# Kernel optimization log

Hardware: AMD Instinct MI355X
Metric: run time of the kernel (lower is better)

The kernel has to match this reference:

```python
import jax, jax.numpy as jnp
import numpy as np

PI = float(np.pi)
C64 = jnp.complex64

# ---- gate matrices (PennyLane conventions) ----

def _rx(t):
    c = jnp.cos(t / 2); s = jnp.sin(t / 2)
    return jnp.array([[c, -1j * s], [-1j * s, c]]).astype(C64)

def _rz(t):
    return jnp.array([[jnp.exp(-0.5j * t), 0.0], [0.0, jnp.exp(0.5j * t)]]).astype(C64)

def _rot(phi, th, om):
    # Rot(phi, theta, omega) = RZ(omega) RY(theta) RZ(phi)
    c = jnp.cos(th / 2); s = jnp.sin(th / 2)
    return jnp.array([
        [jnp.exp(-0.5j * (phi + om)) * c, -jnp.exp(0.5j * (phi - om)) * s],
        [jnp.exp(-0.5j * (phi - om)) * s,  jnp.exp(0.5j * (phi + om)) * c],
    ]).astype(C64)

def _crx(t):
    c = jnp.cos(t / 2); s = jnp.sin(t / 2)
    return jnp.array([
        [1, 0, 0, 0],
        [0, 1, 0, 0],
        [0, 0, c, -1j * s],
        [0, 0, -1j * s, c],
    ]).astype(C64)

CNOT = jnp.array([[1, 0, 0, 0], [0, 1, 0, 0], [0, 0, 0, 1], [0, 0, 1, 0]], dtype=C64)

# ---- state-vector primitives (state shape (2,)*n) ----

def _ap1(psi, U, w):
    return jnp.moveaxis(jnp.tensordot(U, psi, axes=((1,), (w,))), 0, w)

def _ap2(psi, U, a, b):
    U = U.reshape(2, 2, 2, 2)
    return jnp.moveaxis(jnp.tensordot(U, psi, axes=((2, 3), (a, b))), (0, 1), (a, b))

def _expZ(psi, w):
    p = jnp.moveaxis(jnp.abs(psi) ** 2, w, 0)
    return (p[0] - p[1]).sum()

def _expX(psi, w):
    return jnp.real(jnp.sum(jnp.conj(psi) * jnp.flip(psi, axis=w)))

# wire pairs in initQKV_on_wires order
_PAIRS = [(0, 1), (1, 2), (2, 3), (3, 0), (0, 3), (1, 0), (2, 1), (3, 2)]

def _init_qkv(psi, rot_p, crx_p, off):
    for i, (a, b) in enumerate(_PAIRS):
        psi = _ap1(psi, _rot(rot_p[3 * i], rot_p[3 * i + 1], rot_p[3 * i + 2]), off + a)
        psi = _ap2(psi, _crx(crx_p[i]), off + a, off + b)
        psi = _ap2(psi, CNOT, off + a, off + b)
    return psi

def _sample(x, qr, qc, kr, kc, vr, vc):
    # qmha_score: 8-qubit circuit
    psi = jnp.zeros((2,) * 8, C64).at[(0,) * 8].set(1.0)
    for w in range(4):  # AngleEmbedding (RX) of xq
        psi = _ap1(psi, _rx(x[w]), w)
    psi = _init_qkv(psi, qr, qc, 0)
    for w in range(4):  # AngleEmbedding (RX) of xk (same x)
        psi = _ap1(psi, _rx(x[w]), w)
    psi = _init_qkv(psi, kr, kc, 4)
    for w in range(4):
        psi = _ap2(psi, CNOT, w, w + 4)
    z = jnp.stack([_expZ(psi, w) for w in range(4)])
    xm = jnp.stack([_expX(psi, w) for w in range(4)])
    score = jnp.sqrt(z * z + xm * xm)
    # qmha_value: 4-qubit circuit
    phi = jnp.zeros((2,) * 4, C64).at[(0,) * 4].set(1.0)
    for w in range(4):
        phi = _ap1(phi, _rx(x[w]), w)
    phi = _init_qkv(phi, vr, vc, 0)
    for w in range(4):
        phi = _ap1(phi, _rz(jnp.tanh(score[w]) * PI), w)
    for a, b in [(0, 1), (1, 2), (2, 3)]:
        phi = _ap2(phi, CNOT, a, b)
    zv = jnp.stack([_expZ(phi, w) for w in range(4)])
    xv = jnp.stack([_expX(phi, w) for w in range(4)])
    return jnp.concatenate([zv, xv])  # [8]


def setup_inputs() -> dict:
    key = jax.random.key(0)
    ks = jax.random.split(key, 12)
    B = 16384
    u = lambda k, n: jax.random.uniform(k, (n,), jnp.float32, -PI / 2, PI / 2)
    return {
        "x1": jax.random.normal(ks[0], (B, 96), jnp.float32),
        "pre_w": jax.random.normal(ks[1], (4, 96), jnp.float32) / np.sqrt(96.0),
        "pre_b": jnp.zeros((4,), jnp.float32),
        "q_rot": u(ks[2], 24),
        "k_rot": u(ks[3], 24),
        "v_rot": u(ks[4], 24),
        "q_crx": 0.1 * jax.random.normal(ks[5], (8,), jnp.float32),
        "k_crx": 0.1 * jax.random.normal(ks[6], (8,), jnp.float32),
        "v_crx": 0.1 * jax.random.normal(ks[7], (8,), jnp.float32),
        "ln_w": jnp.ones((8,), jnp.float32),
        "ln_b": jnp.zeros((8,), jnp.float32),
        "head_w": jax.random.normal(ks[8], (2, 8), jnp.float32) / np.sqrt(8.0),
        "head_b": jnp.zeros((2,), jnp.float32),
    }


def reference(x1, pre_w, pre_b, q_rot, k_rot, v_rot, q_crx, k_crx, v_crx,
              ln_w, ln_b, head_w, head_b):
    x = x1 @ pre_w.T + pre_b  # [B, 4] angles
    outs = jax.vmap(lambda xi: _sample(xi, q_rot, q_crx, k_rot, k_crx, v_rot, v_crx))(x)  # [B, 8]
    mu = outs.mean(-1, keepdims=True)
    var = outs.var(-1, keepdims=True)
    y = (outs - mu) / jnp.sqrt(var + 1e-5) * ln_w + ln_b  # LayerNorm(8)
    g = jax.nn.gelu(y, approximate=False)  # torch nn.GELU default = exact erf
    return g @ head_w.T + head_b  # [B, 2]
```

## Files before the change

### kernel.cpp

```cpp
#include <hip/hip_runtime.h>
#include <math.h>

#define PI_F 3.14159265358979323846f

struct c32 { float x, y; };


__device__ __forceinline__ void apply_rot_red(c32* s, const int w,
                                              float Ax, float Ay, float Cx, float Cy){
  const int m = 8 >> w;
  #pragma unroll
  for (int i = 0; i < 16; i++){
    if (i & m) continue;
    c32 a = s[i], b = s[i | m];
    s[i].x     = Ax*a.x - Ay*a.y - Cx*b.x - Cy*b.y;
    s[i].y     = Ax*a.y + Ay*a.x - Cx*b.y + Cy*b.x;
    s[i | m].x = Cx*a.x - Cy*a.y + Ax*b.x + Ay*b.y;
    s[i | m].y = Cx*a.y + Cy*a.x + Ax*b.y - Ay*b.x;
  }
}

__device__ __forceinline__ void apply_crxnot(c32* s, const int wa, const int wb,
                                             float c, float sn){
  const int ma = 8 >> wa, mb = 8 >> wb;
  #pragma unroll
  for (int i = 0; i < 16; i++){
    if (!(i & ma) || (i & mb)) continue;
    c32 u = s[i], v = s[i | mb];
    s[i]      = { c*v.x + sn*u.y, c*v.y - sn*u.x };
    s[i | mb] = { c*u.x + sn*v.y, c*u.y - sn*v.x };
  }
}

__device__ __forceinline__ void sim_initqkv(c32* s, const float* gp){
  constexpr int pa[8] = {0,1,2,3,0,1,2,3};
  constexpr int pb[8] = {1,2,3,0,3,0,1,2};
  #pragma unroll
  for (int g = 0; g < 8; g++){
    const float* q = gp + 8*g;
    apply_rot_red(s, pa[g], q[0], q[1], q[2], q[3]);
    apply_crxnot(s, pa[g], pb[g], q[4], q[5]);
  }
}

__device__ __forceinline__ void build_rx(c32* s, const float* cw, const float* sw){
  float m01[4] = { cw[0]*cw[1], cw[0]*sw[1], sw[0]*cw[1], sw[0]*sw[1] };
  float m23[4] = { cw[2]*cw[3], cw[2]*sw[3], sw[2]*cw[3], sw[2]*sw[3] };
  #pragma unroll
  for (int i = 0; i < 16; i++){
    float mag = m01[(i >> 2) & 3] * m23[i & 3];
    const int pc = __popc(i) & 3;
    s[i] = (pc == 0) ? c32{ mag, 0.f } :
           (pc == 1) ? c32{ 0.f, -mag } :
           (pc == 2) ? c32{ -mag, 0.f } : c32{ 0.f, mag };
  }
}

__device__ __forceinline__ float fast_tanh(float x){
  float e = __expf(2.f * x);
  return 1.f - 2.f * __builtin_amdgcn_rcpf(e + 1.f);
}

__global__ __launch_bounds__(64, 1) void qc_setup(
    const float* __restrict__ q_rot, const float* __restrict__ k_rot,
    const float* __restrict__ v_rot,
    const float* __restrict__ q_crx, const float* __restrict__ k_crx,
    const float* __restrict__ v_crx,
    float* __restrict__ ws){

  __shared__ float gates[3 * 64];
  const int t = threadIdx.x;

  if (t < 24){
    const int grp = t >> 3, g = t & 7;
    const float* rotp = grp == 0 ? q_rot : (grp == 1 ? k_rot : v_rot);
    const float* crxp = grp == 0 ? q_crx : (grp == 1 ? k_crx : v_crx);
    float phi = rotp[3*g], th = rotp[3*g+1], om = rotp[3*g+2];
    float c, s, ca, sa, cb, sb;
    __sincosf(0.5f*th,       &s,  &c);
    __sincosf(0.5f*(phi+om), &sa, &ca);
    __sincosf(0.5f*(phi-om), &sb, &cb);
    float cc, cs; __sincosf(0.5f*crxp[g], &cs, &cc);
    float* dst = &gates[64*grp + 8*g];
    dst[0] = c*ca; dst[1] = -c*sa; dst[2] = s*cb; dst[3] = -s*sb;
    dst[4] = cc;   dst[5] = cs;
    dst[6] = 0.f;  dst[7] = 0.f;
  }
  __syncthreads();

  c32 ks[16];
  #pragma unroll
  for (int i = 0; i < 16; i++) ks[i] = { 0.f, 0.f };
  ks[0] = { 1.f, 0.f };
  sim_initqkv(ks, &gates[64]);
  float cxk[4];
  #pragma unroll
  for (int w = 0; w < 4; w++){
    const int m = 8 >> w;
    float r = 0.f;
    #pragma unroll
    for (int i = 0; i < 16; i++){
      if (i & m) continue;
      r += ks[i].x*ks[i|m].x + ks[i].y*ks[i|m].y;
    }
    cxk[w] = 2.f * r;
  }

  ws[t]      = gates[t];
  ws[64 + t] = gates[128 + t];
  if (t < 4) ws[128 + t] = cxk[t];
}

#define LDS_STRIDE 97

__global__ __launch_bounds__(128, 1) void qc_main(
    const float* __restrict__ x1,
    const float* __restrict__ pre_w, const float* __restrict__ pre_b,
    const float* __restrict__ gws,
    const float* __restrict__ ln_w, const float* __restrict__ ln_b,
    const float* __restrict__ head_w, const float* __restrict__ head_b,
    float* __restrict__ out, int B){

  __shared__ float xs[64 * LDS_STRIDE];
  __shared__ float gl[132];
  __shared__ float scr[8][64];

  const int t    = threadIdx.x;
  const int lane = t & 63;
  const int wid  = t >> 6;
  const int base = blockIdx.x * 64;

  if (t < 128) gl[t] = gws[t];
  if (t < 4)   gl[128 + t] = gws[128 + t];

  {
    int rem = B - base; if (rem > 64) rem = 64;
    const int nf4 = rem * 24;
    const float4* src = (const float4*)(x1 + (long)base * 96);
    #pragma unroll
    for (int k = 0; k < 12; k++){
      int g = t + 128*k;
      if (g < nf4){
        float4 v = src[g];
        int f = 4*g;
        int r = f / 96, cidx = f - 96*r;
        float* d = &xs[r*LDS_STRIDE + cidx];
        d[0]=v.x; d[1]=v.y; d[2]=v.z; d[3]=v.w;
      }
    }
  }
  __syncthreads();

  float xw[4];
  {
    float a0 = pre_b[0], a1 = pre_b[1], a2 = pre_b[2], a3 = pre_b[3];
    const float* row = &xs[lane * LDS_STRIDE];
    #pragma unroll
    for (int j = 0; j < 96; j++){
      float v = row[j];
      a0 += v * pre_w[j];
      a1 += v * pre_w[96  + j];
      a2 += v * pre_w[192 + j];
      a3 += v * pre_w[288 + j];
    }
    xw[0]=a0; xw[1]=a1; xw[2]=a2; xw[3]=a3;
  }

  float cw[4], sw[4];
  #pragma unroll
  for (int w = 0; w < 4; w++) __sincosf(0.5f*xw[w], &sw[w], &cw[w]);

  c32 st[16];
  build_rx(st, cw, sw);

  float o[8];

  if (wid == 0){
    sim_initqkv(st, &gl[0]);
    float p[16];
    #pragma unroll
    for (int i = 0; i < 16; i++) p[i] = st[i].x*st[i].x + st[i].y*st[i].y;
    #pragma unroll
    for (int w = 0; w < 4; w++){
      const int m = 8 >> w;
      float sz = 0.f, sx = 0.f, sy = 0.f;
      #pragma unroll
      for (int i = 0; i < 16; i++) sz += (i & m) ? -p[i] : p[i];
      #pragma unroll
      for (int i = 0; i < 16; i++){
        if (i & m) continue;
        c32 a = st[i], b = st[i|m];
        sx += a.x*b.x + a.y*b.y;
        sy += a.x*b.y - a.y*b.x;
      }
      float cth = 1.f - 2.f*sw[w]*sw[w];
      float sth = 2.f*sw[w]*cw[w];
      float z   = cth*sz + sth*(2.f*sy);
      float xm  = (2.f*sx) * gl[128 + w];
      float score = sqrtf(z*z + xm*xm);
      float th = fast_tanh(score) * PI_F;
      float srv, crv; __sincosf(0.5f*th, &srv, &crv);
      scr[2*w][lane]     = crv;
      scr[2*w + 1][lane] = srv;
    }
  } else {
    sim_initqkv(st, &gl[64]);
    float p[16];
    #pragma unroll
    for (int i = 0; i < 16; i++) p[i] = st[i].x*st[i].x + st[i].y*st[i].y;
    constexpr int zm[4] = {8, 12, 14, 15};
    #pragma unroll
    for (int w = 0; w < 4; w++){
      float r = 0.f;
      #pragma unroll
      for (int i = 0; i < 16; i++)
        r += (__popc(i & zm[w]) & 1) ? -p[i] : p[i];
      o[w] = r;
    }
  }

  __syncthreads();

  if (wid == 1){
    float cr[4], sr[4];
    #pragma unroll
    for (int w = 0; w < 4; w++){
      cr[w] = scr[2*w][lane];
      sr[w] = scr[2*w + 1][lane];
    }
    c32 ph01[4], ph23[4];
    ph01[0] = { cr[0]*cr[1] - sr[0]*sr[1], -(cr[0]*sr[1] + sr[0]*cr[1]) };
    ph01[1] = { cr[0]*cr[1] + sr[0]*sr[1],   cr[0]*sr[1] - sr[0]*cr[1] };
    ph01[2] = { ph01[1].x, -ph01[1].y };
    ph01[3] = { ph01[0].x, -ph01[0].y };
    ph23[0] = { cr[2]*cr[3] - sr[2]*sr[3], -(cr[2]*sr[3] + sr[2]*cr[3]) };
    ph23[1] = { cr[2]*cr[3] + sr[2]*sr[3],   cr[2]*sr[3] - sr[2]*cr[3] };
    ph23[2] = { ph23[1].x, -ph23[1].y };
    ph23[3] = { ph23[0].x, -ph23[0].y };
    #pragma unroll
    for (int i = 0; i < 16; i++){
      c32 a = st[i], f = ph01[(i >> 2) & 3], g2 = ph23[i & 3];
      c32 b = { a.x*f.x - a.y*f.y, a.x*f.y + a.y*f.x };
      st[i] = { b.x*g2.x - b.y*g2.y, b.x*g2.y + b.y*g2.x };
    }
    constexpr int xmk[4] = {12, 6, 3, 1};
    constexpr int hb[4]  = {8, 4, 2, 1};
    #pragma unroll
    for (int w = 0; w < 4; w++){
      float r = 0.f;
      #pragma unroll
      for (int i = 0; i < 16; i++){
        if (i & hb[w]) continue;
        const int j = i ^ xmk[w];
        r += st[i].x*st[j].x + st[i].y*st[j].y;
      }
      o[4 + w] = 2.f * r;
    }

    float mu = 0.f;
    #pragma unroll
    for (int j = 0; j < 8; j++) mu += o[j];
    mu *= 0.125f;
    float var = 0.f;
    #pragma unroll
    for (int j = 0; j < 8; j++){ float d = o[j] - mu; var += d*d; }
    var *= 0.125f;
    float inv = rsqrtf(var + 1e-5f);
    float h0 = head_b[0], h1 = head_b[1];
    #pragma unroll
    for (int j = 0; j < 8; j++){
      float y = (o[j] - mu) * inv * ln_w[j] + ln_b[j];
      float u = 0.7978845608f * (y + 0.044715f*y*y*y);
      float g = 0.5f * y * (1.f + fast_tanh(u));
      h0 += g * head_w[j];
      h1 += g * head_w[8 + j];
    }

    const int sid = base + lane;
    if (sid < B){
      float2 r2; r2.x = h0; r2.y = h1;
      ((float2*)out)[sid] = r2;
    }
  }
}

extern "C" void kernel_launch(void* const* d_in, const int* in_sizes, int n_in,
                              void* d_out, int out_size, void* d_ws, size_t ws_size,
                              hipStream_t stream) {
  const float* x1     = (const float*)d_in[0];
  const float* pre_w  = (const float*)d_in[1];
  const float* pre_b  = (const float*)d_in[2];
  const float* q_rot  = (const float*)d_in[3];
  const float* k_rot  = (const float*)d_in[4];
  const float* v_rot  = (const float*)d_in[5];
  const float* q_crx  = (const float*)d_in[6];
  const float* k_crx  = (const float*)d_in[7];
  const float* v_crx  = (const float*)d_in[8];
  const float* ln_w   = (const float*)d_in[9];
  const float* ln_b   = (const float*)d_in[10];
  const float* head_w = (const float*)d_in[11];
  const float* head_b = (const float*)d_in[12];
  float* out = (float*)d_out;
  float* ws  = (float*)d_ws;
  (void)ws_size; (void)n_in; (void)out_size;

  const int B = in_sizes[0] / 96;
  const int nb = (B + 63) / 64;

  qc_setup<<<1, 64, 0, stream>>>(q_rot, k_rot, v_rot, q_crx, k_crx, v_crx, ws);
  qc_main<<<nb, 128, 0, stream>>>(x1, pre_w, pre_b, ws,
                                  ln_w, ln_b, head_w, head_b, out, B);
}
```

Baseline: 93.92 us.

## Split each 4-qubit state across four lanes using DPP cross-lane gate application

The 16-amplitude per-thread state vector is spread over four lanes holding four amplitudes each. Gates on the top two wires are applied through DPP quad permutes, and expectation values are reduced with DPP quad reductions. The pre-projection now splits the 96-element dot product across the quad, reading x1 directly from global memory with weights staged in LDS. Blocks handle 32 samples with 256 threads, so there are more blocks and wavefronts and far fewer registers per thread, at the cost of cross-lane traffic and redundant select logic.

```diff
diff --git a/kernel.cpp b/kernel.cpp
--- a/kernel.cpp
+++ b/kernel.cpp
@@ -5,9 +5,143 @@
 
 struct c32 { float x, y; };
 
-
-__device__ __forceinline__ void apply_rot_red(c32* s, const int w,
-                                              float Ax, float Ay, float Cx, float Cy){
+#define DPP_X1 0xB1
+#define DPP_X2 0x4E
+#define DPP_X3 0x1B
+
+template<int CTRL>
+__device__ __forceinline__ float dppf(float v){
+  return __int_as_float(__builtin_amdgcn_update_dpp(
+      0, __float_as_int(v), CTRL, 0xF, 0xF, true));
+}
+
+__device__ __forceinline__ float qred(float v){
+  v += dppf<DPP_X1>(v);
+  v += dppf<DPP_X2>(v);
+  return v;
+}
+
+__device__ __forceinline__ float sel4(bool b0, bool b1,
+                                      float v0, float v1, float v2, float v3){
+  float lo = b0 ? v1 : v0;
+  float hi = b0 ? v3 : v2;
+  return b1 ? hi : lo;
+}
+
+__device__ __forceinline__ float fast_tanh(float x){
+  float e = __expf(2.f * x);
+  return 1.f - 2.f * __builtin_amdgcn_rcpf(e + 1.f);
+}
+
+
+template<int XM>
+__device__ __forceinline__ void rot_lane(c32* a, float Ax, float Ay,
+                                         float Cx, float Cy, float sgn){
+  c32 r[4];
+  #pragma unroll
+  for (int k = 0; k < 4; k++){ r[k].x = dppf<XM>(a[k].x); r[k].y = dppf<XM>(a[k].y); }
+  float Py = Ay * sgn, Qx = -Cx * sgn;
+  #pragma unroll
+  for (int k = 0; k < 4; k++){
+    float nx = Ax*a[k].x - Py*a[k].y + Qx*r[k].x - Cy*r[k].y;
+    float ny = Ax*a[k].y + Py*a[k].x + Qx*r[k].y + Cy*r[k].x;
+    a[k].x = nx; a[k].y = ny;
+  }
+}
+
+template<int MB>
+__device__ __forceinline__ void rot_local(c32* a, float Ax, float Ay,
+                                          float Cx, float Cy){
+  #pragma unroll
+  for (int k = 0; k < 4; k++){
+    if (k & MB) continue;
+    c32 u = a[k], v = a[k|MB];
+    a[k].x    = Ax*u.x - Ay*u.y - Cx*v.x - Cy*v.y;
+    a[k].y    = Ax*u.y + Ay*u.x - Cx*v.y + Cy*v.x;
+    a[k|MB].x = Cx*u.x - Cy*u.y + Ax*v.x + Ay*v.y;
+    a[k|MB].y = Cx*u.y + Cy*u.x + Ax*v.y - Ay*v.x;
+  }
+}
+
+__device__ __forceinline__ void crx_pair(c32& u, c32& v, float c, float sn){
+  c32 uo = u, vo = v;
+  u.x = c*vo.x + sn*uo.y;  u.y = c*vo.y - sn*uo.x;
+  v.x = c*uo.x + sn*vo.y;  v.y = c*uo.y - sn*vo.x;
+}
+
+template<int KM>
+__device__ __forceinline__ void crx_lanectl_local(c32* a, float c, float sn, bool act){
+  c32 n[4];
+  #pragma unroll
+  for (int k = 0; k < 4; k++){
+    n[k].x = c*a[k^KM].x + sn*a[k].y;
+    n[k].y = c*a[k^KM].y - sn*a[k].x;
+  }
+  #pragma unroll
+  for (int k = 0; k < 4; k++){
+    a[k].x = act ? n[k].x : a[k].x;
+    a[k].y = act ? n[k].y : a[k].y;
+  }
+}
+
+template<int XM, int K0, int K1>
+__device__ __forceinline__ void crx_localctl_lane(c32* a, float c, float sn){
+  float rx0 = dppf<XM>(a[K0].x), ry0 = dppf<XM>(a[K0].y);
+  float rx1 = dppf<XM>(a[K1].x), ry1 = dppf<XM>(a[K1].y);
+  float u0x = a[K0].x, u0y = a[K0].y, u1x = a[K1].x, u1y = a[K1].y;
+  a[K0].x = c*rx0 + sn*u0y;  a[K0].y = c*ry0 - sn*u0x;
+  a[K1].x = c*rx1 + sn*u1y;  a[K1].y = c*ry1 - sn*u1x;
+}
+
+template<int XM>
+__device__ __forceinline__ void crx_lane_lane(c32* a, float c, float sn, bool act){
+  #pragma unroll
+  for (int k = 0; k < 4; k++){
+    float rx = dppf<XM>(a[k].x), ry = dppf<XM>(a[k].y);
+    float nx = c*rx + sn*a[k].y;
+    float ny = c*ry - sn*a[k].x;
+    a[k].x = act ? nx : a[k].x;
+    a[k].y = act ? ny : a[k].y;
+  }
+}
+
+__device__ __forceinline__ void sim4(c32* a, const float* __restrict__ gp,
+                                     float sgnW0, float sgnW1, bool qb0, bool qb1){
+  rot_lane<DPP_X2>(a, gp[0],  gp[1],  gp[2],  gp[3],  sgnW0);
+  crx_lane_lane<DPP_X1>(a, gp[4], gp[5], qb1);
+  rot_lane<DPP_X1>(a, gp[8],  gp[9],  gp[10], gp[11], sgnW1);
+  crx_lanectl_local<2>(a, gp[12], gp[13], qb0);
+  rot_local<2>(a, gp[16], gp[17], gp[18], gp[19]);
+  crx_pair(a[2], a[3], gp[20], gp[21]);
+  rot_local<1>(a, gp[24], gp[25], gp[26], gp[27]);
+  crx_localctl_lane<DPP_X2,1,3>(a, gp[28], gp[29]);
+  rot_lane<DPP_X2>(a, gp[32], gp[33], gp[34], gp[35], sgnW0);
+  crx_lanectl_local<1>(a, gp[36], gp[37], qb1);
+  rot_lane<DPP_X1>(a, gp[40], gp[41], gp[42], gp[43], sgnW1);
+  crx_lane_lane<DPP_X2>(a, gp[44], gp[45], qb0);
+  rot_local<2>(a, gp[48], gp[49], gp[50], gp[51]);
+  crx_localctl_lane<DPP_X1,2,3>(a, gp[52], gp[53]);
+  rot_local<1>(a, gp[56], gp[57], gp[58], gp[59]);
+  crx_pair(a[1], a[3], gp[60], gp[61]);
+}
+
+__device__ __forceinline__ void build_rx4(c32* a, const float* cw, const float* sw,
+                                          int q, bool qb0, bool qb1){
+  float m01 = (qb1 ? sw[0] : cw[0]) * (qb0 ? sw[1] : cw[1]);
+  float g0 = m01 * (cw[2]*cw[3]);
+  float g1 = m01 * (cw[2]*sw[3]);
+  float g2 = m01 * (sw[2]*cw[3]);
+  float g3 = m01 * (sw[2]*sw[3]);
+  float bx = (q == 0) ? 1.f : (q == 3) ? -1.f : 0.f;
+  float by = (q == 1 || q == 2) ? -1.f : 0.f;
+  a[0].x =  g0*bx;  a[0].y =  g0*by;
+  a[1].x =  g1*by;  a[1].y = -g1*bx;
+  a[2].x =  g2*by;  a[2].y = -g2*bx;
+  a[3].x = -g3*bx;  a[3].y = -g3*by;
+}
+
+__device__ __forceinline__ void apply_rot_red16(c32* s, const int w,
+                                                float Ax, float Ay, float Cx, float Cy){
   const int m = 8 >> w;
   #pragma unroll
   for (int i = 0; i < 16; i++){
@@ -20,8 +154,8 @@
   }
 }
 
-__device__ __forceinline__ void apply_crxnot(c32* s, const int wa, const int wb,
-                                             float c, float sn){
+__device__ __forceinline__ void apply_crxnot16(c32* s, const int wa, const int wb,
+                                               float c, float sn){
   const int ma = 8 >> wa, mb = 8 >> wb;
   #pragma unroll
   for (int i = 0; i < 16; i++){
@@ -30,35 +164,6 @@
     s[i]      = { c*v.x + sn*u.y, c*v.y - sn*u.x };
     s[i | mb] = { c*u.x + sn*v.y, c*u.y - sn*v.x };
   }
-}
-
-__device__ __forceinline__ void sim_initqkv(c32* s, const float* gp){
-  constexpr int pa[8] = {0,1,2,3,0,1,2,3};
-  constexpr int pb[8] = {1,2,3,0,3,0,1,2};
-  #pragma unroll
-  for (int g = 0; g < 8; g++){
-    const float* q = gp + 8*g;
-    apply_rot_red(s, pa[g], q[0], q[1], q[2], q[3]);
-    apply_crxnot(s, pa[g], pb[g], q[4], q[5]);
-  }
-}
-
-__device__ __forceinline__ void build_rx(c32* s, const float* cw, const float* sw){
-  float m01[4] = { cw[0]*cw[1], cw[0]*sw[1], sw[0]*cw[1], sw[0]*sw[1] };
-  float m23[4] = { cw[2]*cw[3], cw[2]*sw[3], sw[2]*cw[3], sw[2]*sw[3] };
-  #pragma unroll
-  for (int i = 0; i < 16; i++){
-    float mag = m01[(i >> 2) & 3] * m23[i & 3];
-    const int pc = __popc(i) & 3;
-    s[i] = (pc == 0) ? c32{ mag, 0.f } :
-           (pc == 1) ? c32{ 0.f, -mag } :
-           (pc == 2) ? c32{ -mag, 0.f } : c32{ 0.f, mag };
-  }
-}
-
-__device__ __forceinline__ float fast_tanh(float x){
-  float e = __expf(2.f * x);
-  return 1.f - 2.f * __builtin_amdgcn_rcpf(e + 1.f);
 }
 
 __global__ __launch_bounds__(64, 1) void qc_setup(
@@ -92,7 +197,16 @@
   #pragma unroll
   for (int i = 0; i < 16; i++) ks[i] = { 0.f, 0.f };
   ks[0] = { 1.f, 0.f };
-  sim_initqkv(ks, &gates[64]);
+  {
+    constexpr int pa[8] = {0,1,2,3,0,1,2,3};
+    constexpr int pb[8] = {1,2,3,0,3,0,1,2};
+    #pragma unroll
+    for (int g = 0; g < 8; g++){
+      const float* qq = &gates[64 + 8*g];
+      apply_rot_red16(ks, pa[g], qq[0], qq[1], qq[2], qq[3]);
+      apply_crxnot16(ks, pa[g], pb[g], qq[4], qq[5]);
+    }
+  }
   float cxk[4];
   #pragma unroll
   for (int w = 0; w < 4; w++){
@@ -111,9 +225,7 @@
   if (t < 4) ws[128 + t] = cxk[t];
 }
 
-#define LDS_STRIDE 97
-
-__global__ __launch_bounds__(128, 1) void qc_main(
+__global__ __launch_bounds__(256, 1) void qc_main(
     const float* __restrict__ x1,
     const float* __restrict__ pre_w, const float* __restrict__ pre_b,
     const float* __restrict__ gws,
@@ -121,142 +233,169 @@
     const float* __restrict__ head_w, const float* __restrict__ head_b,
     float* __restrict__ out, int B){
 
-  __shared__ float xs[64 * LDS_STRIDE];
-  __shared__ float gl[132];
-  __shared__ float scr[8][64];
+  __shared__ float pw[4][100];
+  __shared__ float scr[32][9];
 
   const int t    = threadIdx.x;
   const int lane = t & 63;
   const int wid  = t >> 6;
-  const int base = blockIdx.x * 64;
-
-  if (t < 128) gl[t] = gws[t];
-  if (t < 4)   gl[128 + t] = gws[128 + t];
-
-  {
-    int rem = B - base; if (rem > 64) rem = 64;
-    const int nf4 = rem * 24;
-    const float4* src = (const float4*)(x1 + (long)base * 96);
-    #pragma unroll
-    for (int k = 0; k < 12; k++){
-      int g = t + 128*k;
-      if (g < nf4){
-        float4 v = src[g];
-        int f = 4*g;
-        int r = f / 96, cidx = f - 96*r;
-        float* d = &xs[r*LDS_STRIDE + cidx];
-        d[0]=v.x; d[1]=v.y; d[2]=v.z; d[3]=v.w;
-      }
-    }
+  const bool qrole = (wid & 1) == 0;
+  const int sm   = (wid >> 1) * 16 + (lane >> 2);
+  const int q    = lane & 3;
+  const bool qb0 = (q & 1) != 0;
+  const bool qb1 = (q & 2) != 0;
+  const int sid  = blockIdx.x * 32 + sm;
+  const int sidc = (sid < B) ? sid : (B - 1);
+
+  if (t < 96){
+    float4 v = ((const float4*)pre_w)[t];
+    int r = t / 24, c4 = (t % 24) * 4;
+    pw[r][c4+0] = v.x; pw[r][c4+1] = v.y; pw[r][c4+2] = v.z; pw[r][c4+3] = v.w;
   }
   __syncthreads();
 
   float xw[4];
   {
-    float a0 = pre_b[0], a1 = pre_b[1], a2 = pre_b[2], a3 = pre_b[3];
-    const float* row = &xs[lane * LDS_STRIDE];
-    #pragma unroll
-    for (int j = 0; j < 96; j++){
-      float v = row[j];
-      a0 += v * pre_w[j];
-      a1 += v * pre_w[96  + j];
-      a2 += v * pre_w[192 + j];
-      a3 += v * pre_w[288 + j];
-    }
-    xw[0]=a0; xw[1]=a1; xw[2]=a2; xw[3]=a3;
+    float a0 = 0.f, a1 = 0.f, a2 = 0.f, a3 = 0.f;
+    const float4* xrow = (const float4*)(x1 + (size_t)sidc * 96 + 24*q);
+    #pragma unroll
+    for (int j = 0; j < 6; j++){
+      float4 xv = xrow[j];
+      const int c = 24*q + 4*j;
+      float4 w0 = *(const float4*)&pw[0][c];
+      float4 w1 = *(const float4*)&pw[1][c];
+      float4 w2 = *(const float4*)&pw[2][c];
+      float4 w3 = *(const float4*)&pw[3][c];
+      a0 += xv.x*w0.x + xv.y*w0.y + xv.z*w0.z + xv.w*w0.w;
+      a1 += xv.x*w1.x + xv.y*w1.y + xv.z*w1.z + xv.w*w1.w;
+      a2 += xv.x*w2.x + xv.y*w2.y + xv.z*w2.z + xv.w*w2.w;
+      a3 += xv.x*w3.x + xv.y*w3.y + xv.z*w3.z + xv.w*w3.w;
+    }
+    xw[0] = qred(a0) + pre_b[0];
+    xw[1] = qred(a1) + pre_b[1];
+    xw[2] = qred(a2) + pre_b[2];
+    xw[3] = qred(a3) + pre_b[3];
   }
 
   float cw[4], sw[4];
   #pragma unroll
   for (int w = 0; w < 4; w++) __sincosf(0.5f*xw[w], &sw[w], &cw[w]);
 
-  c32 st[16];
-  build_rx(st, cw, sw);
-
-  float o[8];
-
-  if (wid == 0){
-    sim_initqkv(st, &gl[0]);
-    float p[16];
-    #pragma unroll
-    for (int i = 0; i < 16; i++) p[i] = st[i].x*st[i].x + st[i].y*st[i].y;
-    #pragma unroll
-    for (int w = 0; w < 4; w++){
-      const int m = 8 >> w;
-      float sz = 0.f, sx = 0.f, sy = 0.f;
-      #pragma unroll
-      for (int i = 0; i < 16; i++) sz += (i & m) ? -p[i] : p[i];
-      #pragma unroll
-      for (int i = 0; i < 16; i++){
-        if (i & m) continue;
-        c32 a = st[i], b = st[i|m];
-        sx += a.x*b.x + a.y*b.y;
-        sy += a.x*b.y - a.y*b.x;
-      }
-      float cth = 1.f - 2.f*sw[w]*sw[w];
-      float sth = 2.f*sw[w]*cw[w];
-      float z   = cth*sz + sth*(2.f*sy);
-      float xm  = (2.f*sx) * gl[128 + w];
-      float score = sqrtf(z*z + xm*xm);
-      float th = fast_tanh(score) * PI_F;
-      float srv, crv; __sincosf(0.5f*th, &srv, &crv);
-      scr[2*w][lane]     = crv;
-      scr[2*w + 1][lane] = srv;
-    }
+  const float sgnW0 = qb1 ? -1.f : 1.f;
+  const float sgnW1 = qb0 ? -1.f : 1.f;
+
+  c32 a[4];
+  build_rx4(a, cw, sw, q, qb0, qb1);
+
+  float o0, o1, o2, o3;
+
+  if (qrole){
+    sim4(a, gws, sgnW0, sgnW1, qb0, qb1);
+
+    float p0 = a[0].x*a[0].x + a[0].y*a[0].y;
+    float p1 = a[1].x*a[1].x + a[1].y*a[1].y;
+    float p2 = a[2].x*a[2].x + a[2].y*a[2].y;
+    float p3 = a[3].x*a[3].x + a[3].y*a[3].y;
+    float psum = p0 + p1 + p2 + p3;
+
+    float sz2 = p0 + p1 - p2 - p3;
+    float sx2 = 2.f*(a[0].x*a[2].x + a[0].y*a[2].y + a[1].x*a[3].x + a[1].y*a[3].y);
+    float sy2 = 2.f*(a[0].x*a[2].y - a[0].y*a[2].x + a[1].x*a[3].y - a[1].y*a[3].x);
+    float sz3 = p0 - p1 + p2 - p3;
+    float sx3 = 2.f*(a[0].x*a[1].x + a[0].y*a[1].y + a[2].x*a[3].x + a[2].y*a[3].y);
+    float sy3 = 2.f*(a[0].x*a[1].y - a[0].y*a[1].x + a[2].x*a[3].y - a[2].y*a[3].x);
+
+    c32 r[4];
+    #pragma unroll
+    for (int k = 0; k < 4; k++){ r[k].x = dppf<DPP_X2>(a[k].x); r[k].y = dppf<DPP_X2>(a[k].y); }
+    float sx0 = a[0].x*r[0].x + a[0].y*r[0].y + a[1].x*r[1].x + a[1].y*r[1].y
+              + a[2].x*r[2].x + a[2].y*r[2].y + a[3].x*r[3].x + a[3].y*r[3].y;
+    float sy0 = (a[0].x*r[0].y - a[0].y*r[0].x + a[1].x*r[1].y - a[1].y*r[1].x
+               + a[2].x*r[2].y - a[2].y*r[2].x + a[3].x*r[3].y - a[3].y*r[3].x) * sgnW0;
+    float sz0 = sgnW0 * psum;
+
+    #pragma unroll
+    for (int k = 0; k < 4; k++){ r[k].x = dppf<DPP_X1>(a[k].x); r[k].y = dppf<DPP_X1>(a[k].y); }
+    float sx1 = a[0].x*r[0].x + a[0].y*r[0].y + a[1].x*r[1].x + a[1].y*r[1].y
+              + a[2].x*r[2].x + a[2].y*r[2].y + a[3].x*r[3].x + a[3].y*r[3].y;
+    float sy1 = (a[0].x*r[0].y - a[0].y*r[0].x + a[1].x*r[1].y - a[1].y*r[1].x
+               + a[2].x*r[2].y - a[2].y*r[2].x + a[3].x*r[3].y - a[3].y*r[3].x) * sgnW1;
+    float sz1 = sgnW1 * psum;
+
+    sz0 = qred(sz0); sx0 = qred(sx0); sy0 = qred(sy0);
+    sz1 = qred(sz1); sx1 = qred(sx1); sy1 = qred(sy1);
+    sz2 = qred(sz2); sx2 = qred(sx2); sy2 = qred(sy2);
+    sz3 = qred(sz3); sx3 = qred(sx3); sy3 = qred(sy3);
+
+    float szq = sel4(qb0, qb1, sz0, sz1, sz2, sz3);
+    float sxq = sel4(qb0, qb1, sx0, sx1, sx2, sx3);
+    float syq = sel4(qb0, qb1, sy0, sy1, sy2, sy3);
+    float swq = sel4(qb0, qb1, sw[0], sw[1], sw[2], sw[3]);
+    float cwq = sel4(qb0, qb1, cw[0], cw[1], cw[2], cw[3]);
+    float cxkq = sel4(qb0, qb1, gws[128], gws[129], gws[130], gws[131]);
+
+    float cth = 1.f - 2.f*swq*swq;
+    float sth = 2.f*swq*cwq;
+    float z   = cth*szq + sth*syq;
+    float xm  = sxq * cxkq;
+    float score = sqrtf(z*z + xm*xm);
+    float th = fast_tanh(score) * PI_F;
+    float srv, crv; __sincosf(0.5f*th, &srv, &crv);
+    scr[sm][2*q]     = crv;
+    scr[sm][2*q + 1] = srv;
   } else {
-    sim_initqkv(st, &gl[64]);
-    float p[16];
-    #pragma unroll
-    for (int i = 0; i < 16; i++) p[i] = st[i].x*st[i].x + st[i].y*st[i].y;
-    constexpr int zm[4] = {8, 12, 14, 15};
-    #pragma unroll
-    for (int w = 0; w < 4; w++){
-      float r = 0.f;
-      #pragma unroll
-      for (int i = 0; i < 16; i++)
-        r += (__popc(i & zm[w]) & 1) ? -p[i] : p[i];
-      o[w] = r;
-    }
+    sim4(a, gws + 64, sgnW0, sgnW1, qb0, qb1);
+
+    float p0 = a[0].x*a[0].x + a[0].y*a[0].y;
+    float p1 = a[1].x*a[1].x + a[1].y*a[1].y;
+    float p2 = a[2].x*a[2].x + a[2].y*a[2].y;
+    float p3 = a[3].x*a[3].x + a[3].y*a[3].y;
+    float psum = p0 + p1 + p2 + p3;
+    float sgn01 = sgnW0 * sgnW1;
+    o0 = qred(sgnW0 * psum);
+    o1 = qred(sgn01 * psum);
+    o2 = qred(sgn01 * (p0 + p1 - p2 - p3));
+    o3 = qred(sgn01 * (p0 - p1 - p2 + p3));
   }
 
   __syncthreads();
 
-  if (wid == 1){
-    float cr[4], sr[4];
-    #pragma unroll
-    for (int w = 0; w < 4; w++){
-      cr[w] = scr[2*w][lane];
-      sr[w] = scr[2*w + 1][lane];
-    }
-    c32 ph01[4], ph23[4];
-    ph01[0] = { cr[0]*cr[1] - sr[0]*sr[1], -(cr[0]*sr[1] + sr[0]*cr[1]) };
-    ph01[1] = { cr[0]*cr[1] + sr[0]*sr[1],   cr[0]*sr[1] - sr[0]*cr[1] };
-    ph01[2] = { ph01[1].x, -ph01[1].y };
-    ph01[3] = { ph01[0].x, -ph01[0].y };
-    ph23[0] = { cr[2]*cr[3] - sr[2]*sr[3], -(cr[2]*sr[3] + sr[2]*cr[3]) };
-    ph23[1] = { cr[2]*cr[3] + sr[2]*sr[3],   cr[2]*sr[3] - sr[2]*cr[3] };
-    ph23[2] = { ph23[1].x, -ph23[1].y };
-    ph23[3] = { ph23[0].x, -ph23[0].y };
-    #pragma unroll
-    for (int i = 0; i < 16; i++){
-      c32 a = st[i], f = ph01[(i >> 2) & 3], g2 = ph23[i & 3];
-      c32 b = { a.x*f.x - a.y*f.y, a.x*f.y + a.y*f.x };
-      st[i] = { b.x*g2.x - b.y*g2.y, b.x*g2.y + b.y*g2.x };
-    }
-    constexpr int xmk[4] = {12, 6, 3, 1};
-    constexpr int hb[4]  = {8, 4, 2, 1};
-    #pragma unroll
-    for (int w = 0; w < 4; w++){
-      float r = 0.f;
-      #pragma unroll
-      for (int i = 0; i < 16; i++){
-        if (i & hb[w]) continue;
-        const int j = i ^ xmk[w];
-        r += st[i].x*st[j].x + st[i].y*st[j].y;
-      }
-      o[4 + w] = 2.f * r;
-    }
-
+  if (!qrole){
+    float c0 = scr[sm][0], s0 = scr[sm][1];
+    float c1 = scr[sm][2], s1 = scr[sm][3];
+    float c2 = scr[sm][4], s2 = scr[sm][5];
+    float c3 = scr[sm][6], s3 = scr[sm][7];
+
+    float c01m = c0*c1 - s0*s1, c01p = c0*c1 + s0*s1;
+    float s01p = c0*s1 + s0*c1, s01m = c0*s1 - s0*c1;
+    bool selq = qb0 != qb1;
+    float phx = selq ? c01p : c01m;
+    float phm = selq ? s01m : s01p;
+    float phy = qb0 ? phm : -phm;
+    float c23m = c2*c3 - s2*s3, c23p = c2*c3 + s2*s3;
+    float s23p = c2*s3 + s2*c3, s23m = c2*s3 - s2*c3;
+    c32 P[4] = { {c23m, -s23p}, {c23p, s23m}, {c23p, -s23m}, {c23m, s23p} };
+    #pragma unroll
+    for (int k = 0; k < 4; k++){
+      c32 b = { a[k].x*phx - a[k].y*phy, a[k].x*phy + a[k].y*phx };
+      a[k].x = b.x*P[k].x - b.y*P[k].y;
+      a[k].y = b.x*P[k].y + b.y*P[k].x;
+    }
+
+    c32 r[4];
+    #pragma unroll
+    for (int k = 0; k < 4; k++){ r[k].x = dppf<DPP_X3>(a[k].x); r[k].y = dppf<DPP_X3>(a[k].y); }
+    float s4 = a[0].x*r[0].x + a[0].y*r[0].y + a[1].x*r[1].x + a[1].y*r[1].y
+             + a[2].x*r[2].x + a[2].y*r[2].y + a[3].x*r[3].x + a[3].y*r[3].y;
+    #pragma unroll
+    for (int k = 0; k < 4; k++){ r[k].x = dppf<DPP_X1>(a[k].x); r[k].y = dppf<DPP_X1>(a[k].y); }
+    float s5 = a[0].x*r[2].x + a[0].y*r[2].y + a[1].x*r[3].x + a[1].y*r[3].y
+             + a[2].x*r[0].x + a[2].y*r[0].y + a[3].x*r[1].x + a[3].y*r[1].y;
+    float s6 = 2.f*(a[0].x*a[3].x + a[0].y*a[3].y + a[1].x*a[2].x + a[1].y*a[2].y);
+    float s7 = 2.f*(a[0].x*a[1].x + a[0].y*a[1].y + a[2].x*a[3].x + a[2].y*a[3].y);
+    float o4 = qred(s4), o5 = qred(s5), o6 = qred(s6), o7 = qred(s7);
+
+    float o[8] = { o0, o1, o2, o3, o4, o5, o6, o7 };
     float mu = 0.f;
     #pragma unroll
     for (int j = 0; j < 8; j++) mu += o[j];
@@ -276,8 +415,7 @@
       h1 += g * head_w[8 + j];
     }
 
-    const int sid = base + lane;
-    if (sid < B){
+    if (q == 0 && sid < B){
       float2 r2; r2.x = h0; r2.y = h1;
       ((float2*)out)[sid] = r2;
     }
@@ -305,9 +443,9 @@
   (void)ws_size; (void)n_in; (void)out_size;
 
   const int B = in_sizes[0] / 96;
-  const int nb = (B + 63) / 64;
+  const int nb = (B + 31) / 32;
 
   qc_setup<<<1, 64, 0, stream>>>(q_rot, k_rot, v_rot, q_crx, k_crx, v_crx, ws);
-  qc_main<<<nb, 128, 0, stream>>>(x1, pre_w, pre_b, ws,
+  qc_main<<<nb, 256, 0, stream>>>(x1, pre_w, pre_b, ws,
                                   ln_w, ln_b, head_w, head_b, out, B);
 }
```

Result: faster. 89.37 us (-4.8%).
